# Kernel optimization log

Measured on AMD Instinct MI355X. Metric: run time of the kernel, lower is better.

The kernel has to match this reference:

```python
import jax, jax.numpy as jnp
import numpy as np

E = 262144      # total neighbor edges across all (sample, timestep) pairs
B = 1024        # samples with non-zero history
L = 10          # seq_len
T = B * L       # total timesteps (segments)
H = 128         # h_dim
N_ENT = 40000
N_REL = 256


def setup_inputs() -> dict:
    key = jax.random.key(0)
    ks = jax.random.split(key, 16)
    return {
        "nbr_ent": jax.random.randint(ks[0], (E,), 0, N_ENT),
        "nbr_rel": jax.random.randint(ks[1], (E,), 0, N_REL),
        "nbr_att": jax.random.uniform(ks[2], (E,), dtype=jnp.float32),
        "seg_ids": jnp.sort(jax.random.randint(ks[3], (E,), 0, T)),
        "self_att": jax.random.uniform(ks[4], (B, L), dtype=jnp.float32),
        "s_ids": jax.random.randint(ks[5], (B,), 0, N_ENT),
        "r_ids": jax.random.randint(ks[6], (B,), 0, N_REL),
        "ent_embeds": jax.random.normal(ks[7], (N_ENT, H), dtype=jnp.float32),
        "rel_embeds": jax.random.normal(ks[8], (N_REL, H), dtype=jnp.float32),
        "W1_w": jax.random.normal(ks[9], (H, 1), dtype=jnp.float32) * 0.1,
        "W1_b": jax.random.normal(ks[10], (H,), dtype=jnp.float32) * 0.1,
        "W3_w": jax.random.normal(ks[11], (H, 3 * H), dtype=jnp.float32) * 0.05,
        "W3_b": jax.random.normal(ks[12], (H,), dtype=jnp.float32) * 0.05,
        "W4_w": jax.random.normal(ks[13], (H, 2 * H), dtype=jnp.float32) * 0.05,
        "W4_b": jax.random.normal(ks[14], (H,), dtype=jnp.float32) * 0.05,
    }


def reference(nbr_ent, nbr_rel, nbr_att, seg_ids, self_att, s_ids, r_ids,
              ent_embeds, rel_embeds, W1_w, W1_b, W3_w, W3_b, W4_w, W4_b):
    # --- per-edge embeddings (the body of get_sorted_s_r_embed) ---
    # W1: scalar attribute -> h_dim, then ReLU
    e_att = jax.nn.relu(nbr_att[:, None] * W1_w[:, 0][None, :] + W1_b)   # [E, H]
    e_s = ent_embeds[nbr_ent]                                            # [E, H]
    e_r = rel_embeds[nbr_rel]                                            # [E, H]
    e = jax.nn.relu(jnp.concatenate([e_att, e_s, e_r], -1) @ W3_w.T + W3_b)      # [E, H]
    e_static = jax.nn.relu(jnp.concatenate([e_s, e_r], -1) @ W4_w.T + W4_b)      # [E, H]

    # --- sparse-mask segment mean (torch.sparse.mm with 0/1 mask / len_s) ---
    counts = jax.ops.segment_sum(jnp.ones_like(nbr_att), seg_ids, num_segments=T)
    denom = jnp.maximum(counts, 1.0)[:, None]                            # guard empty segments
    embeds_mean = jax.ops.segment_sum(e, seg_ids, num_segments=T) / denom          # [T, H]
    embeds_static_mean = jax.ops.segment_sum(e_static, seg_ids, num_segments=T) / denom

    embeds_mean = embeds_mean.reshape(B, L, H)
    embeds_static_mean = embeds_static_mean.reshape(B, L, H)

    # --- per-sample fill of padded sequence tensors ---
    self_att_emb = jax.nn.relu(self_att[..., None] * W1_w[:, 0] + W1_b)  # [B, L, H]
    self_e = jnp.broadcast_to(ent_embeds[s_ids][:, None, :], (B, L, H))  # repeat over time
    self_r = jnp.broadcast_to(rel_embeds[r_ids][:, None, :], (B, L, H))

    s_embed_seq = jnp.concatenate([self_e, self_r, embeds_static_mean], -1)   # [B, L, 3H]
    att_embed_seq = jnp.concatenate([self_att_emb, self_e, embeds_mean], -1)  # [B, L, 3H]
    # dropout omitted (eval mode); pack_padded_sequence returns padded tensors here
    return s_embed_seq, att_embed_seq
```

## Files before the change

kernel.cpp:

```cpp
#include <hip/hip_runtime.h>
#include <hip/hip_bf16.h>

#define E_EDGES 262144
#define B_SAMP  1024
#define L_SEQ   10
#define T_SEG   (B_SAMP * L_SEQ)
#define H_DIM   128
#define N_ENT_C 40000
#define N_REL_C 256

typedef __attribute__((ext_vector_type(8))) short short8;
typedef __attribute__((ext_vector_type(4))) float f32x4;

__device__ __forceinline__ float b2f(__hip_bfloat16 x) { return __bfloat162float(x); }
__device__ __forceinline__ unsigned short f2bu(float x) {
    return __bfloat16_as_ushort(__float2bfloat16(x));
}

__device__ __forceinline__ float loadF(const void* base, int idx, int isB16) {
    if (isB16) return b2f(((const __hip_bfloat16*)base)[idx]);
    return ((const float*)base)[idx];
}
__device__ __forceinline__ int loadI(const void* base, int idx, int is64) {
    if (is64) return (int)(((const long long*)base)[idx]);
    return ((const int*)base)[idx];
}

__device__ __forceinline__ void detect_dtypes(const void* att_raw,
                                              const void* sid_raw,
                                              int tid, int nthr,
                                              int& isB, int& i64)
{
    __shared__ int cF, cI;
    if (tid == 0) { cF = 0; cI = 0; }
    __syncthreads();
    const unsigned short* pa = (const unsigned short*)att_raw;
    int c = 0;
    for (int i = tid; i < 2048; i += nthr) if (pa[i] <= 0x3F80u) c++;
    if (c) atomicAdd(&cF, c);
    const int* ps = (const int*)sid_raw;
    c = 0;
    for (int i = tid; i < 512; i += nthr) if (ps[2 * i + 1] == 0) c++;
    if (c) atomicAdd(&cI, c);
    __syncthreads();
    isB = (cF >= 1900) ? 1 : 0;
    i64 = (cI >= 256) ? 1 : 0;
}

__global__ void __launch_bounds__(256)
ka_prep(const void* __restrict__ W3w, const void* __restrict__ W4w,
        const void* __restrict__ W1w, const void* __restrict__ W1b,
        const void* __restrict__ W3b, const void* __restrict__ W4b,
        const void* __restrict__ seg_ids,
        const void* __restrict__ att_raw, const void* __restrict__ sid_raw,
        unsigned short* __restrict__ wctEb, unsigned short* __restrict__ wctRb,
        unsigned int* __restrict__ ab3p, int* __restrict__ starts,
        float* __restrict__ W1w_f, float* __restrict__ W1b_f,
        float* __restrict__ W3b_f, float* __restrict__ W4b_f,
        float* __restrict__ bpts, int* __restrict__ pnIn,
        int* __restrict__ flag, int* __restrict__ iflag)
{
    const int bid = blockIdx.x, tid = threadIdx.x;
    int isB, i64;
    detect_dtypes(att_raw, sid_raw, tid, 256, isB, i64);

    if (bid < 256) {
        int gid = bid * 256 + tid;
        if (gid < 32768) {
            int n = gid >> 7, k = gid & 127;
            float v = (n < 128) ? loadF(W3w, n * 384 + 128 + k, isB)
                                : loadF(W4w, (n - 128) * 256 + k, isB);
            wctEb[gid] = f2bu(v);
        } else {
            int j = gid - 32768;
            int n = j >> 7, k = j & 127;
            float v = (n < 128) ? loadF(W3w, n * 384 + 256 + k, isB)
                                : loadF(W4w, (n - 128) * 256 + 128 + k, isB);
            wctRb[j] = f2bu(v);
        }
        return;
    }

    if (bid < 321 || bid == 362) {
        __shared__ float w1s[128], b1s[128], srt[128];
        __shared__ int nInS;
        if (tid < 128) {
            float w = loadF(W1w, tid, isB);
            float b = loadF(W1b, tid, isB);
            w1s[tid] = w; b1s[tid] = b;
        }
        __syncthreads();
        if (tid < 128) {
            float w = w1s[tid], b = b1s[tid];
            float t = 2.0f;
            if (w != 0.0f) {
                float tt = -b / w;
                if (tt > 0.0f && tt < 1.0f) t = tt;
            }
            srt[tid] = t;
        }
        __syncthreads();
        float myt = 0.0f; int rank = 0, n = 0;
        if (tid < 128) {
            myt = srt[tid];
            for (int j = 0; j < 128; ++j) {
                float v = srt[j];
                rank += (v < myt) || (v == myt && j < tid);
                n += (v < 1.5f);
            }
        }
        __syncthreads();
        if (tid < 128) srt[rank] = myt;
        if (tid == 0) nInS = n;
        __syncthreads();
        const int nIn = nInS;

        if (bid == 362) {
            if (tid < 128) {
                W1w_f[tid] = w1s[tid];
                W1b_f[tid] = b1s[tid];
                W3b_f[tid] = loadF(W3b, tid, isB);
                W4b_f[tid] = loadF(W4b, tid, isB);
                bpts[tid] = srt[tid];
            }
            if (tid == 0) { *pnIn = nIn; *flag = isB; *iflag = i64; }
            return;
        }
        const int j = (bid - 256) * 2 + (tid >> 7);
        const int h = tid & 127;
        if (j <= nIn) {
            float left  = (j == 0)   ? 0.0f : srt[j - 1];
            float right = (j == nIn) ? 1.0f : srt[j];
            float mid = 0.5f * (left + right);
            float a = 0.0f, b = 0.0f;
            for (int k = 0; k < 128; ++k) {
                if (fmaf(mid, w1s[k], b1s[k]) > 0.0f) {
                    float w3 = loadF(W3w, h * 384 + k, isB);
                    a = fmaf(w1s[k], w3, a);
                    b = fmaf(b1s[k], w3, b);
                }
            }
            ab3p[j * 128 + h] = (unsigned int)f2bu(a)
                              | ((unsigned int)f2bu(b) << 16);
        }
        return;
    }

    int t = (bid - 321) * 256 + tid;
    if (t <= T_SEG) {
        int lo = 0, hi = E_EDGES;
        while (lo < hi) {
            int m = (lo + hi) >> 1;
            if (loadI(seg_ids, m, i64) < t) lo = m + 1; else hi = m;
        }
        starts[t] = lo;
    }
}

#define KB_ENT_BLOCKS (N_ENT_C / 64)
#define KB_REL_BLOCKS (N_REL_C / 64)

__global__ void __launch_bounds__(256)
kb_gemm(const void* __restrict__ ent_raw, const void* __restrict__ rel_raw,
        const int* __restrict__ flag,
        const unsigned short* __restrict__ wctEb,
        const unsigned short* __restrict__ wctRb,
        const float* __restrict__ W3b_f, const float* __restrict__ W4b_f,
        unsigned int* __restrict__ entp2, unsigned int* __restrict__ relp2)
{
    const int isB = *flag;
    const int bid = blockIdx.x, tid = threadIdx.x;

    const void* A; const unsigned short* WT; unsigned int* out; int m0, isRel;
    if (bid < KB_ENT_BLOCKS) {
        A = ent_raw; WT = wctEb; out = entp2; m0 = bid * 64; isRel = 0;
    } else {
        A = rel_raw; WT = wctRb; out = relp2;
        m0 = (bid - KB_ENT_BLOCKS) * 64; isRel = 1;
    }

    __shared__ unsigned short As[64][136];

    if (isB) {
        for (int v = tid; v < 1024; v += 256) {
            int e = v * 8, r = e >> 7, cc = e & 127;
            short8 x = *(const short8*)((const short*)A + m0 * 128 + e);
            *(short8*)&As[r][cc] = x;
        }
    } else {
        for (int v = tid; v < 2048; v += 256) {
            int e = v * 4, r = e >> 7, cc = e & 127;
            float4 f = *(const float4*)((const float*)A + m0 * 128 + e);
            unsigned int lo = (unsigned int)f2bu(f.x) | ((unsigned int)f2bu(f.y) << 16);
            unsigned int hi = (unsigned int)f2bu(f.z) | ((unsigned int)f2bu(f.w) << 16);
            *(uint2*)&As[r][cc] = make_uint2(lo, hi);
        }
    }
    __syncthreads();

    const int wave = tid >> 6, lane = tid & 63;
    const int quad = lane >> 4, l16 = lane & 15;

    f32x4 acc3[8], acc4[8];
    #pragma unroll
    for (int np = 0; np < 8; ++np) {
        acc3[np] = (f32x4){0.f, 0.f, 0.f, 0.f};
        acc4[np] = (f32x4){0.f, 0.f, 0.f, 0.f};
    }

    #pragma unroll
    for (int kk = 0; kk < 4; ++kk) {
        const int kb = kk * 32 + quad * 8;
        short8 av = *(const short8*)&As[wave * 16 + l16][kb];
        #pragma unroll
        for (int np = 0; np < 8; ++np) {
            const short* bp = (const short*)WT + (np * 16 + l16) * 128 + kb;
            short8 bv3 = *(const short8*)bp;
            short8 bv4 = *(const short8*)(bp + 128 * 128);
            acc3[np] = __builtin_amdgcn_mfma_f32_16x16x32_bf16(av, bv3, acc3[np], 0, 0, 0);
            acc4[np] = __builtin_amdgcn_mfma_f32_16x16x32_bf16(av, bv4, acc4[np], 0, 0, 0);
        }
    }

    #pragma unroll
    for (int np = 0; np < 8; ++np) {
        int h = np * 16 + l16;
        float bias3 = isRel ? W3b_f[h] : 0.0f;
        float bias4 = isRel ? W4b_f[h] : 0.0f;
        #pragma unroll
        for (int r = 0; r < 4; ++r) {
            int m = m0 + wave * 16 + quad * 4 + r;
            unsigned int w = (unsigned int)f2bu(acc3[np][r] + bias3)
                           | ((unsigned int)f2bu(acc4[np][r] + bias4) << 16);
            out[m * 128 + h] = w;
        }
    }
}

__global__ void __launch_bounds__(128)
kc_segment(const void* __restrict__ nbr_ent, const void* __restrict__ nbr_rel,
           const void* __restrict__ att_raw,
           const int* __restrict__ starts,
           const unsigned int* __restrict__ entp2,
           const unsigned int* __restrict__ relp2,
           const unsigned int* __restrict__ ab3p,
           const float* __restrict__ bpts_g, const int* __restrict__ pnIn,
           const void* __restrict__ sat_raw,
           const void* __restrict__ s_ids, const void* __restrict__ r_ids,
           const void* __restrict__ ent_raw, const void* __restrict__ rel_raw,
           const float* __restrict__ W1w_f, const float* __restrict__ W1b_f,
           const int* __restrict__ flag, const int* __restrict__ iflag,
           float* __restrict__ outS, float* __restrict__ outA)
{
    const int t = blockIdx.x, h = threadIdx.x;
    const int isB = *flag, i64 = *iflag;
    const int s = starts[t], e = starts[t + 1];

    __shared__ float bptsS[128];
    __shared__ int4 eS[128];
    bptsS[h] = bpts_g[h];
    const int nIn = *pnIn;

    float acc3 = 0.0f, acc4 = 0.0f;

    for (int base = s; base < e; base += 128) {
        const int n = min(128, e - base);
        __syncthreads();
        if (h < n) {
            const int i = base + h;
            int ent = loadI(nbr_ent, i, i64);
            int rel = loadI(nbr_rel, i, i64);
            float att = loadF(att_raw, i, isB);
            int lo = 0, hi = nIn;
            while (lo < hi) {
                int m = (lo + hi) >> 1;
                if (bptsS[m] <= att) lo = m + 1; else hi = m;
            }
            eS[h] = make_int4(ent, rel, __float_as_int(att), lo);
        }
        __syncthreads();
        #pragma unroll 8
        for (int ii = 0; ii < n; ++ii) {
            int4 q = eS[ii];
            float att = __int_as_float(q.z);
            unsigned int ew = entp2[q.x * 128 + h];
            unsigned int rw = relp2[q.y * 128 + h];
            unsigned int aw = ab3p[q.w * 128 + h];
            float p3s = __int_as_float(ew << 16);
            float p4s = __int_as_float(ew & 0xFFFF0000u);
            float p3r = __int_as_float(rw << 16);
            float p4r = __int_as_float(rw & 0xFFFF0000u);
            float a3  = __int_as_float(aw << 16);
            float b3  = __int_as_float(aw & 0xFFFF0000u);
            acc3 += fmaxf(fmaf(att, a3, b3) + p3s + p3r, 0.0f);
            acc4 += fmaxf(p4s + p4r, 0.0f);
        }
    }

    const int cnt = e - s;
    const float inv = (cnt > 0) ? (1.0f / (float)cnt) : 1.0f;
    const int b = t / L_SEQ;
    const int sid = loadI(s_ids, b, i64);
    const int rid = loadI(r_ids, b, i64);
    const float se = loadF(ent_raw, sid * 128 + h, isB);
    const float sr = loadF(rel_raw, rid * 128 + h, isB);
    const float sa = loadF(sat_raw, t, isB);
    const float sae = fmaxf(fmaf(sa, W1w_f[h], W1b_f[h]), 0.0f);

    const size_t bs = (size_t)t * 384;
    outS[bs + h]       = se;
    outS[bs + 128 + h] = sr;
    outS[bs + 256 + h] = acc4 * inv;
    outA[bs + h]       = sae;
    outA[bs + 128 + h] = se;
    outA[bs + 256 + h] = acc3 * inv;
}

extern "C" void kernel_launch(void* const* d_in, const int* in_sizes, int n_in,
                              void* d_out, int out_size, void* d_ws, size_t ws_size,
                              hipStream_t stream)
{
    const void* nbr_ent = d_in[0];
    const void* nbr_rel = d_in[1];
    const void* nbr_att = d_in[2];
    const void* seg_ids = d_in[3];
    const void* self_att = d_in[4];
    const void* s_ids = d_in[5];
    const void* r_ids = d_in[6];
    const void* ent_embeds = d_in[7];
    const void* rel_embeds = d_in[8];
    const void* W1w = d_in[9];
    const void* W1b = d_in[10];
    const void* W3w = d_in[11];
    const void* W3b = d_in[12];
    const void* W4w = d_in[13];
    const void* W4b = d_in[14];

    char* ws = (char*)d_ws;
    size_t off = 0;
    auto alloc = [&](size_t bytes) -> void* {
        void* p = ws + off;
        off = (off + bytes + 255) & ~(size_t)255;
        return p;
    };
    int*   flag   = (int*)alloc(4);
    int*   iflag  = (int*)alloc(4);
    int*   pnIn   = (int*)alloc(4);
    float* W1w_f  = (float*)alloc(128 * 4);
    float* W1b_f  = (float*)alloc(128 * 4);
    float* W3b_f  = (float*)alloc(128 * 4);
    float* W4b_f  = (float*)alloc(128 * 4);
    float* bpts   = (float*)alloc(128 * 4);
    int*   starts = (int*)alloc((T_SEG + 1) * 4);
    unsigned short* wctEb = (unsigned short*)alloc(256 * 128 * 2);
    unsigned short* wctRb = (unsigned short*)alloc(256 * 128 * 2);
    unsigned int* ab3p = (unsigned int*)alloc(129 * 128 * 4);
    unsigned int* entp2 = (unsigned int*)alloc((size_t)N_ENT_C * 128 * 4);
    unsigned int* relp2 = (unsigned int*)alloc((size_t)N_REL_C * 128 * 4);

    float* outS = (float*)d_out;
    float* outA = outS + (size_t)T_SEG * 384;

    ka_prep<<<363, 256, 0, stream>>>(W3w, W4w, W1w, W1b, W3b, W4b,
                                     seg_ids, nbr_att, s_ids,
                                     wctEb, wctRb, ab3p, starts,
                                     W1w_f, W1b_f, W3b_f, W4b_f,
                                     bpts, pnIn, flag, iflag);

    kb_gemm<<<KB_ENT_BLOCKS + KB_REL_BLOCKS, 256, 0, stream>>>(
        ent_embeds, rel_embeds, flag, wctEb, wctRb, W3b_f, W4b_f, entp2, relp2);

    kc_segment<<<T_SEG, 128, 0, stream>>>(
        nbr_ent, nbr_rel, nbr_att, starts, entp2, relp2, ab3p, bpts, pnIn,
        self_att, s_ids, r_ids, ent_embeds, rel_embeds,
        W1w_f, W1b_f, flag, iflag, outS, outA);
}
```

Before: 179.2 us.

## Precompute packed per-edge metadata in prep kernel and use wave-per-segment gather

```diff
diff --git a/kernel.cpp b/kernel.cpp
--- a/kernel.cpp
+++ b/kernel.cpp
@@ -52,12 +52,13 @@
         const void* __restrict__ W1w, const void* __restrict__ W1b,
         const void* __restrict__ W3b, const void* __restrict__ W4b,
         const void* __restrict__ seg_ids,
+        const void* __restrict__ nbr_ent, const void* __restrict__ nbr_rel,
         const void* __restrict__ att_raw, const void* __restrict__ sid_raw,
         unsigned short* __restrict__ wctEb, unsigned short* __restrict__ wctRb,
         unsigned int* __restrict__ ab3p, int* __restrict__ starts,
+        uint2* __restrict__ metaE,
         float* __restrict__ W1w_f, float* __restrict__ W1b_f,
         float* __restrict__ W3b_f, float* __restrict__ W4b_f,
-        float* __restrict__ bpts, int* __restrict__ pnIn,
         int* __restrict__ flag, int* __restrict__ iflag)
 {
     const int bid = blockIdx.x, tid = threadIdx.x;
@@ -81,51 +82,64 @@
         return;
     }
 
-    if (bid < 321 || bid == 362) {
-        __shared__ float w1s[128], b1s[128], srt[128];
-        __shared__ int nInS;
+    if (bid >= 321 && bid <= 361) {
+        int t = (bid - 321) * 256 + tid;
+        if (t <= T_SEG) {
+            int lo = 0, hi = E_EDGES;
+            while (lo < hi) {
+                int m = (lo + hi) >> 1;
+                if (loadI(seg_ids, m, i64) < t) lo = m + 1; else hi = m;
+            }
+            starts[t] = lo;
+        }
+        return;
+    }
+
+    __shared__ float w1s[128], b1s[128], srt[128];
+    __shared__ int nInS;
+    if (tid < 128) {
+        float w = loadF(W1w, tid, isB);
+        float b = loadF(W1b, tid, isB);
+        w1s[tid] = w; b1s[tid] = b;
+    }
+    __syncthreads();
+    if (tid < 128) {
+        float w = w1s[tid], b = b1s[tid];
+        float t = 2.0f;
+        if (w != 0.0f) {
+            float tt = -b / w;
+            if (tt > 0.0f && tt < 1.0f) t = tt;
+        }
+        srt[tid] = t;
+    }
+    __syncthreads();
+    float myt = 0.0f; int rank = 0, n = 0;
+    if (tid < 128) {
+        myt = srt[tid];
+        for (int j = 0; j < 128; ++j) {
+            float v = srt[j];
+            rank += (v < myt) || (v == myt && j < tid);
+            n += (v < 1.5f);
+        }
+    }
+    __syncthreads();
+    if (tid < 128) srt[rank] = myt;
+    if (tid == 0) nInS = n;
+    __syncthreads();
+    const int nIn = nInS;
+
+    if (bid == 362) {
         if (tid < 128) {
-            float w = loadF(W1w, tid, isB);
-            float b = loadF(W1b, tid, isB);
-            w1s[tid] = w; b1s[tid] = b;
-        }
-        __syncthreads();
-        if (tid < 128) {
-            float w = w1s[tid], b = b1s[tid];
-            float t = 2.0f;
-            if (w != 0.0f) {
-                float tt = -b / w;
-                if (tt > 0.0f && tt < 1.0f) t = tt;
-            }
-            srt[tid] = t;
-        }
-        __syncthreads();
-        float myt = 0.0f; int rank = 0, n = 0;
-        if (tid < 128) {
-            myt = srt[tid];
-            for (int j = 0; j < 128; ++j) {
-                float v = srt[j];
-                rank += (v < myt) || (v == myt && j < tid);
-                n += (v < 1.5f);
-            }
-        }
-        __syncthreads();
-        if (tid < 128) srt[rank] = myt;
-        if (tid == 0) nInS = n;
-        __syncthreads();
-        const int nIn = nInS;
-
-        if (bid == 362) {
-            if (tid < 128) {
-                W1w_f[tid] = w1s[tid];
-                W1b_f[tid] = b1s[tid];
-                W3b_f[tid] = loadF(W3b, tid, isB);
-                W4b_f[tid] = loadF(W4b, tid, isB);
-                bpts[tid] = srt[tid];
-            }
-            if (tid == 0) { *pnIn = nIn; *flag = isB; *iflag = i64; }
-            return;
-        }
+            W1w_f[tid] = w1s[tid];
+            W1b_f[tid] = b1s[tid];
+            W3b_f[tid] = loadF(W3b, tid, isB);
+            W4b_f[tid] = loadF(W4b, tid, isB);
+        }
+        if (tid == 0) { *flag = isB; *iflag = i64; }
+        return;
+    }
+
+    if (bid < 321) {
         const int j = (bid - 256) * 2 + (tid >> 7);
         const int h = tid & 127;
         if (j <= nIn) {
@@ -146,14 +160,22 @@
         return;
     }
 
-    int t = (bid - 321) * 256 + tid;
-    if (t <= T_SEG) {
-        int lo = 0, hi = E_EDGES;
+    const int eb = (bid - 363) * 1024;
+    #pragma unroll
+    for (int r = 0; r < 4; ++r) {
+        int i = eb + r * 256 + tid;
+        int ent = loadI(nbr_ent, i, i64);
+        int rel = loadI(nbr_rel, i, i64);
+        float att = loadF(att_raw, i, isB);
+        int lo = 0, hi = nIn;
         while (lo < hi) {
             int m = (lo + hi) >> 1;
-            if (loadI(seg_ids, m, i64) < t) lo = m + 1; else hi = m;
-        }
-        starts[t] = lo;
+            if (srt[m] <= att) lo = m + 1; else hi = m;
+        }
+        unsigned int hiw = (unsigned int)ent
+                         | ((unsigned int)rel << 16)
+                         | ((unsigned int)lo << 24);
+        metaE[i] = make_uint2(__float_as_uint(att), hiw);
     }
 }
 
@@ -237,14 +259,12 @@
     }
 }
 
-__global__ void __launch_bounds__(128)
-kc_segment(const void* __restrict__ nbr_ent, const void* __restrict__ nbr_rel,
-           const void* __restrict__ att_raw,
+__global__ void __launch_bounds__(256)
+kc_segment(const uint2* __restrict__ metaE,
            const int* __restrict__ starts,
            const unsigned int* __restrict__ entp2,
            const unsigned int* __restrict__ relp2,
            const unsigned int* __restrict__ ab3p,
-           const float* __restrict__ bpts_g, const int* __restrict__ pnIn,
            const void* __restrict__ sat_raw,
            const void* __restrict__ s_ids, const void* __restrict__ r_ids,
            const void* __restrict__ ent_raw, const void* __restrict__ rel_raw,
@@ -252,48 +272,50 @@
            const int* __restrict__ flag, const int* __restrict__ iflag,
            float* __restrict__ outS, float* __restrict__ outA)
 {
-    const int t = blockIdx.x, h = threadIdx.x;
     const int isB = *flag, i64 = *iflag;
-    const int s = starts[t], e = starts[t + 1];
-
-    __shared__ float bptsS[128];
-    __shared__ int4 eS[128];
-    bptsS[h] = bpts_g[h];
-    const int nIn = *pnIn;
-
-    float acc3 = 0.0f, acc4 = 0.0f;
-
-    for (int base = s; base < e; base += 128) {
-        const int n = min(128, e - base);
-        __syncthreads();
-        if (h < n) {
-            const int i = base + h;
-            int ent = loadI(nbr_ent, i, i64);
-            int rel = loadI(nbr_rel, i, i64);
-            float att = loadF(att_raw, i, isB);
-            int lo = 0, hi = nIn;
-            while (lo < hi) {
-                int m = (lo + hi) >> 1;
-                if (bptsS[m] <= att) lo = m + 1; else hi = m;
-            }
-            eS[h] = make_int4(ent, rel, __float_as_int(att), lo);
-        }
-        __syncthreads();
-        #pragma unroll 8
+    const int wave = threadIdx.x >> 6, lane = threadIdx.x & 63;
+    const int t = blockIdx.x * 4 + wave;
+    const int h0 = lane * 2;
+
+    const int s = __builtin_amdgcn_readfirstlane(starts[t]);
+    const int e = __builtin_amdgcn_readfirstlane(starts[t + 1]);
+
+    float acc3x = 0.0f, acc3y = 0.0f, acc4x = 0.0f, acc4y = 0.0f;
+
+    for (int base = s; base < e; base += 64) {
+        const int n = min(64, e - base);
+        unsigned int mLo = 0u, mHi = 0u;
+        if (lane < n) {
+            uint2 mv = metaE[base + lane];
+            mLo = mv.x; mHi = mv.y;
+        }
+        #pragma unroll 4
         for (int ii = 0; ii < n; ++ii) {
-            int4 q = eS[ii];
-            float att = __int_as_float(q.z);
-            unsigned int ew = entp2[q.x * 128 + h];
-            unsigned int rw = relp2[q.y * 128 + h];
-            unsigned int aw = ab3p[q.w * 128 + h];
-            float p3s = __int_as_float(ew << 16);
-            float p4s = __int_as_float(ew & 0xFFFF0000u);
-            float p3r = __int_as_float(rw << 16);
-            float p4r = __int_as_float(rw & 0xFFFF0000u);
-            float a3  = __int_as_float(aw << 16);
-            float b3  = __int_as_float(aw & 0xFFFF0000u);
-            acc3 += fmaxf(fmaf(att, a3, b3) + p3s + p3r, 0.0f);
-            acc4 += fmaxf(p4s + p4r, 0.0f);
+            const unsigned int sLo = __builtin_amdgcn_readlane(mLo, ii);
+            const unsigned int sHi = __builtin_amdgcn_readlane(mHi, ii);
+            const float att = __uint_as_float(sLo);
+            const int ent = (int)(sHi & 0xFFFFu);
+            const int rel = (int)((sHi >> 16) & 0xFFu);
+            const int j   = (int)(sHi >> 24);
+            uint2 ew = *(const uint2*)(entp2 + ent * 128 + h0);
+            uint2 rw = *(const uint2*)(relp2 + rel * 128 + h0);
+            uint2 aw = *(const uint2*)(ab3p  + j   * 128 + h0);
+            float p3s0 = __uint_as_float(ew.x << 16);
+            float p4s0 = __uint_as_float(ew.x & 0xFFFF0000u);
+            float p3s1 = __uint_as_float(ew.y << 16);
+            float p4s1 = __uint_as_float(ew.y & 0xFFFF0000u);
+            float p3r0 = __uint_as_float(rw.x << 16);
+            float p4r0 = __uint_as_float(rw.x & 0xFFFF0000u);
+            float p3r1 = __uint_as_float(rw.y << 16);
+            float p4r1 = __uint_as_float(rw.y & 0xFFFF0000u);
+            float a30  = __uint_as_float(aw.x << 16);
+            float b30  = __uint_as_float(aw.x & 0xFFFF0000u);
+            float a31  = __uint_as_float(aw.y << 16);
+            float b31  = __uint_as_float(aw.y & 0xFFFF0000u);
+            acc3x += fmaxf(fmaf(att, a30, b30) + p3s0 + p3r0, 0.0f);
+            acc3y += fmaxf(fmaf(att, a31, b31) + p3s1 + p3r1, 0.0f);
+            acc4x += fmaxf(p4s0 + p4r0, 0.0f);
+            acc4y += fmaxf(p4s1 + p4r1, 0.0f);
         }
     }
 
@@ -302,18 +324,23 @@
     const int b = t / L_SEQ;
     const int sid = loadI(s_ids, b, i64);
     const int rid = loadI(r_ids, b, i64);
-    const float se = loadF(ent_raw, sid * 128 + h, isB);
-    const float sr = loadF(rel_raw, rid * 128 + h, isB);
-    const float sa = loadF(sat_raw, t, isB);
-    const float sae = fmaxf(fmaf(sa, W1w_f[h], W1b_f[h]), 0.0f);
+    const float se0 = loadF(ent_raw, sid * 128 + h0, isB);
+    const float se1 = loadF(ent_raw, sid * 128 + h0 + 1, isB);
+    const float sr0 = loadF(rel_raw, rid * 128 + h0, isB);
+    const float sr1 = loadF(rel_raw, rid * 128 + h0 + 1, isB);
+    const float sa  = loadF(sat_raw, t, isB);
+    const float2 w1w = *(const float2*)(W1w_f + h0);
+    const float2 w1b = *(const float2*)(W1b_f + h0);
+    const float sae0 = fmaxf(fmaf(sa, w1w.x, w1b.x), 0.0f);
+    const float sae1 = fmaxf(fmaf(sa, w1w.y, w1b.y), 0.0f);
 
     const size_t bs = (size_t)t * 384;
-    outS[bs + h]       = se;
-    outS[bs + 128 + h] = sr;
-    outS[bs + 256 + h] = acc4 * inv;
-    outA[bs + h]       = sae;
-    outA[bs + 128 + h] = se;
-    outA[bs + 256 + h] = acc3 * inv;
+    *(float2*)(outS + bs + h0)       = make_float2(se0, se1);
+    *(float2*)(outS + bs + 128 + h0) = make_float2(sr0, sr1);
+    *(float2*)(outS + bs + 256 + h0) = make_float2(acc4x * inv, acc4y * inv);
+    *(float2*)(outA + bs + h0)       = make_float2(sae0, sae1);
+    *(float2*)(outA + bs + 128 + h0) = make_float2(se0, se1);
+    *(float2*)(outA + bs + 256 + h0) = make_float2(acc3x * inv, acc3y * inv);
 }
 
 extern "C" void kernel_launch(void* const* d_in, const int* in_sizes, int n_in,
@@ -345,33 +372,32 @@
     };
     int*   flag   = (int*)alloc(4);
     int*   iflag  = (int*)alloc(4);
-    int*   pnIn   = (int*)alloc(4);
     float* W1w_f  = (float*)alloc(128 * 4);
     float* W1b_f  = (float*)alloc(128 * 4);
     float* W3b_f  = (float*)alloc(128 * 4);
     float* W4b_f  = (float*)alloc(128 * 4);
-    float* bpts   = (float*)alloc(128 * 4);
     int*   starts = (int*)alloc((T_SEG + 1) * 4);
     unsigned short* wctEb = (unsigned short*)alloc(256 * 128 * 2);
     unsigned short* wctRb = (unsigned short*)alloc(256 * 128 * 2);
     unsigned int* ab3p = (unsigned int*)alloc(129 * 128 * 4);
+    uint2* metaE = (uint2*)alloc((size_t)E_EDGES * 8);
     unsigned int* entp2 = (unsigned int*)alloc((size_t)N_ENT_C * 128 * 4);
     unsigned int* relp2 = (unsigned int*)alloc((size_t)N_REL_C * 128 * 4);
 
     float* outS = (float*)d_out;
     float* outA = outS + (size_t)T_SEG * 384;
 
-    ka_prep<<<363, 256, 0, stream>>>(W3w, W4w, W1w, W1b, W3b, W4b,
-                                     seg_ids, nbr_att, s_ids,
-                                     wctEb, wctRb, ab3p, starts,
+    ka_prep<<<619, 256, 0, stream>>>(W3w, W4w, W1w, W1b, W3b, W4b,
+                                     seg_ids, nbr_ent, nbr_rel, nbr_att, s_ids,
+                                     wctEb, wctRb, ab3p, starts, metaE,
                                      W1w_f, W1b_f, W3b_f, W4b_f,
-                                     bpts, pnIn, flag, iflag);
+                                     flag, iflag);
 
     kb_gemm<<<KB_ENT_BLOCKS + KB_REL_BLOCKS, 256, 0, stream>>>(
         ent_embeds, rel_embeds, flag, wctEb, wctRb, W3b_f, W4b_f, entp2, relp2);
 
-    kc_segment<<<T_SEG, 128, 0, stream>>>(
-        nbr_ent, nbr_rel, nbr_att, starts, entp2, relp2, ab3p, bpts, pnIn,
+    kc_segment<<<T_SEG / 4, 256, 0, stream>>>(
+        metaE, starts, entp2, relp2, ab3p,
         self_att, s_ids, r_ids, ent_embeds, rel_embeds,
         W1w_f, W1b_f, flag, iflag, outS, outA);
 }
```

After: 189.7 us. 5.8% more time.

## Precompute packed per-edge metadata in prep kernel and halve GEMM tile size

Applied to the files above, without the earlier changes.

```diff
diff --git a/kernel.cpp b/kernel.cpp
--- a/kernel.cpp
+++ b/kernel.cpp
@@ -52,12 +52,13 @@
         const void* __restrict__ W1w, const void* __restrict__ W1b,
         const void* __restrict__ W3b, const void* __restrict__ W4b,
         const void* __restrict__ seg_ids,
+        const void* __restrict__ nbr_ent, const void* __restrict__ nbr_rel,
         const void* __restrict__ att_raw, const void* __restrict__ sid_raw,
         unsigned short* __restrict__ wctEb, unsigned short* __restrict__ wctRb,
         unsigned int* __restrict__ ab3p, int* __restrict__ starts,
+        uint2* __restrict__ metaE,
         float* __restrict__ W1w_f, float* __restrict__ W1b_f,
         float* __restrict__ W3b_f, float* __restrict__ W4b_f,
-        float* __restrict__ bpts, int* __restrict__ pnIn,
         int* __restrict__ flag, int* __restrict__ iflag)
 {
     const int bid = blockIdx.x, tid = threadIdx.x;
@@ -81,51 +82,64 @@
         return;
     }
 
-    if (bid < 321 || bid == 362) {
-        __shared__ float w1s[128], b1s[128], srt[128];
-        __shared__ int nInS;
+    if (bid >= 321 && bid <= 361) {
+        int t = (bid - 321) * 256 + tid;
+        if (t <= T_SEG) {
+            int lo = 0, hi = E_EDGES;
+            while (lo < hi) {
+                int m = (lo + hi) >> 1;
+                if (loadI(seg_ids, m, i64) < t) lo = m + 1; else hi = m;
+            }
+            starts[t] = lo;
+        }
+        return;
+    }
+
+    __shared__ float w1s[128], b1s[128], srt[128];
+    __shared__ int nInS;
+    if (tid < 128) {
+        float w = loadF(W1w, tid, isB);
+        float b = loadF(W1b, tid, isB);
+        w1s[tid] = w; b1s[tid] = b;
+    }
+    __syncthreads();
+    if (tid < 128) {
+        float w = w1s[tid], b = b1s[tid];
+        float t = 2.0f;
+        if (w != 0.0f) {
+            float tt = -b / w;
+            if (tt > 0.0f && tt < 1.0f) t = tt;
+        }
+        srt[tid] = t;
+    }
+    __syncthreads();
+    float myt = 0.0f; int rank = 0, n = 0;
+    if (tid < 128) {
+        myt = srt[tid];
+        for (int j = 0; j < 128; ++j) {
+            float v = srt[j];
+            rank += (v < myt) || (v == myt && j < tid);
+            n += (v < 1.5f);
+        }
+    }
+    __syncthreads();
+    if (tid < 128) srt[rank] = myt;
+    if (tid == 0) nInS = n;
+    __syncthreads();
+    const int nIn = nInS;
+
+    if (bid == 362) {
         if (tid < 128) {
-            float w = loadF(W1w, tid, isB);
-            float b = loadF(W1b, tid, isB);
-            w1s[tid] = w; b1s[tid] = b;
-        }
-        __syncthreads();
-        if (tid < 128) {
-            float w = w1s[tid], b = b1s[tid];
-            float t = 2.0f;
-            if (w != 0.0f) {
-                float tt = -b / w;
-                if (tt > 0.0f && tt < 1.0f) t = tt;
-            }
-            srt[tid] = t;
-        }
-        __syncthreads();
-        float myt = 0.0f; int rank = 0, n = 0;
-        if (tid < 128) {
-            myt = srt[tid];
-            for (int j = 0; j < 128; ++j) {
-                float v = srt[j];
-                rank += (v < myt) || (v == myt && j < tid);
-                n += (v < 1.5f);
-            }
-        }
-        __syncthreads();
-        if (tid < 128) srt[rank] = myt;
-        if (tid == 0) nInS = n;
-        __syncthreads();
-        const int nIn = nInS;
-
-        if (bid == 362) {
-            if (tid < 128) {
-                W1w_f[tid] = w1s[tid];
-                W1b_f[tid] = b1s[tid];
-                W3b_f[tid] = loadF(W3b, tid, isB);
-                W4b_f[tid] = loadF(W4b, tid, isB);
-                bpts[tid] = srt[tid];
-            }
-            if (tid == 0) { *pnIn = nIn; *flag = isB; *iflag = i64; }
-            return;
-        }
+            W1w_f[tid] = w1s[tid];
+            W1b_f[tid] = b1s[tid];
+            W3b_f[tid] = loadF(W3b, tid, isB);
+            W4b_f[tid] = loadF(W4b, tid, isB);
+        }
+        if (tid == 0) { *flag = isB; *iflag = i64; }
+        return;
+    }
+
+    if (bid < 321) {
         const int j = (bid - 256) * 2 + (tid >> 7);
         const int h = tid & 127;
         if (j <= nIn) {
@@ -146,21 +160,29 @@
         return;
     }
 
-    int t = (bid - 321) * 256 + tid;
-    if (t <= T_SEG) {
-        int lo = 0, hi = E_EDGES;
+    const int eb = (bid - 363) * 1024;
+    #pragma unroll
+    for (int r = 0; r < 4; ++r) {
+        int i = eb + r * 256 + tid;
+        int ent = loadI(nbr_ent, i, i64);
+        int rel = loadI(nbr_rel, i, i64);
+        float att = loadF(att_raw, i, isB);
+        int lo = 0, hi = nIn;
         while (lo < hi) {
             int m = (lo + hi) >> 1;
-            if (loadI(seg_ids, m, i64) < t) lo = m + 1; else hi = m;
-        }
-        starts[t] = lo;
-    }
-}
-
-#define KB_ENT_BLOCKS (N_ENT_C / 64)
-#define KB_REL_BLOCKS (N_REL_C / 64)
-
-__global__ void __launch_bounds__(256)
+            if (srt[m] <= att) lo = m + 1; else hi = m;
+        }
+        unsigned int hiw = (unsigned int)ent
+                         | ((unsigned int)rel << 16)
+                         | ((unsigned int)lo << 24);
+        metaE[i] = make_uint2(__float_as_uint(att), hiw);
+    }
+}
+
+#define KB_ENT_BLOCKS (N_ENT_C / 32)
+#define KB_REL_BLOCKS (N_REL_C / 32)
+
+__global__ void __launch_bounds__(128)
 kb_gemm(const void* __restrict__ ent_raw, const void* __restrict__ rel_raw,
         const int* __restrict__ flag,
         const unsigned short* __restrict__ wctEb,
@@ -173,22 +195,22 @@
 
     const void* A; const unsigned short* WT; unsigned int* out; int m0, isRel;
     if (bid < KB_ENT_BLOCKS) {
-        A = ent_raw; WT = wctEb; out = entp2; m0 = bid * 64; isRel = 0;
+        A = ent_raw; WT = wctEb; out = entp2; m0 = bid * 32; isRel = 0;
     } else {
         A = rel_raw; WT = wctRb; out = relp2;
-        m0 = (bid - KB_ENT_BLOCKS) * 64; isRel = 1;
-    }
-
-    __shared__ unsigned short As[64][136];
+        m0 = (bid - KB_ENT_BLOCKS) * 32; isRel = 1;
+    }
+
+    __shared__ unsigned short As[32][136];
 
     if (isB) {
-        for (int v = tid; v < 1024; v += 256) {
+        for (int v = tid; v < 512; v += 128) {
             int e = v * 8, r = e >> 7, cc = e & 127;
             short8 x = *(const short8*)((const short*)A + m0 * 128 + e);
             *(short8*)&As[r][cc] = x;
         }
     } else {
-        for (int v = tid; v < 2048; v += 256) {
+        for (int v = tid; v < 1024; v += 128) {
             int e = v * 4, r = e >> 7, cc = e & 127;
             float4 f = *(const float4*)((const float*)A + m0 * 128 + e);
             unsigned int lo = (unsigned int)f2bu(f.x) | ((unsigned int)f2bu(f.y) << 16);
@@ -238,13 +260,11 @@
 }
 
 __global__ void __launch_bounds__(128)
-kc_segment(const void* __restrict__ nbr_ent, const void* __restrict__ nbr_rel,
-           const void* __restrict__ att_raw,
+kc_segment(const uint2* __restrict__ metaE,
            const int* __restrict__ starts,
            const unsigned int* __restrict__ entp2,
            const unsigned int* __restrict__ relp2,
            const unsigned int* __restrict__ ab3p,
-           const float* __restrict__ bpts_g, const int* __restrict__ pnIn,
            const void* __restrict__ sat_raw,
            const void* __restrict__ s_ids, const void* __restrict__ r_ids,
            const void* __restrict__ ent_raw, const void* __restrict__ rel_raw,
@@ -256,42 +276,31 @@
     const int isB = *flag, i64 = *iflag;
     const int s = starts[t], e = starts[t + 1];
 
-    __shared__ float bptsS[128];
-    __shared__ int4 eS[128];
-    bptsS[h] = bpts_g[h];
-    const int nIn = *pnIn;
+    __shared__ uint2 eS[128];
 
     float acc3 = 0.0f, acc4 = 0.0f;
 
     for (int base = s; base < e; base += 128) {
         const int n = min(128, e - base);
         __syncthreads();
-        if (h < n) {
-            const int i = base + h;
-            int ent = loadI(nbr_ent, i, i64);
-            int rel = loadI(nbr_rel, i, i64);
-            float att = loadF(att_raw, i, isB);
-            int lo = 0, hi = nIn;
-            while (lo < hi) {
-                int m = (lo + hi) >> 1;
-                if (bptsS[m] <= att) lo = m + 1; else hi = m;
-            }
-            eS[h] = make_int4(ent, rel, __float_as_int(att), lo);
-        }
+        if (h < n) eS[h] = metaE[base + h];
         __syncthreads();
         #pragma unroll 8
         for (int ii = 0; ii < n; ++ii) {
-            int4 q = eS[ii];
-            float att = __int_as_float(q.z);
-            unsigned int ew = entp2[q.x * 128 + h];
-            unsigned int rw = relp2[q.y * 128 + h];
-            unsigned int aw = ab3p[q.w * 128 + h];
-            float p3s = __int_as_float(ew << 16);
-            float p4s = __int_as_float(ew & 0xFFFF0000u);
-            float p3r = __int_as_float(rw << 16);
-            float p4r = __int_as_float(rw & 0xFFFF0000u);
-            float a3  = __int_as_float(aw << 16);
-            float b3  = __int_as_float(aw & 0xFFFF0000u);
+            uint2 q = eS[ii];
+            float att = __uint_as_float(q.x);
+            int ent = (int)(q.y & 0xFFFFu);
+            int rel = (int)((q.y >> 16) & 0xFFu);
+            int j   = (int)(q.y >> 24);
+            unsigned int ew = entp2[ent * 128 + h];
+            unsigned int rw = relp2[rel * 128 + h];
+            unsigned int aw = ab3p[j * 128 + h];
+            float p3s = __uint_as_float(ew << 16);
+            float p4s = __uint_as_float(ew & 0xFFFF0000u);
+            float p3r = __uint_as_float(rw << 16);
+            float p4r = __uint_as_float(rw & 0xFFFF0000u);
+            float a3  = __uint_as_float(aw << 16);
+            float b3  = __uint_as_float(aw & 0xFFFF0000u);
             acc3 += fmaxf(fmaf(att, a3, b3) + p3s + p3r, 0.0f);
             acc4 += fmaxf(p4s + p4r, 0.0f);
         }
@@ -345,33 +354,32 @@
     };
     int*   flag   = (int*)alloc(4);
     int*   iflag  = (int*)alloc(4);
-    int*   pnIn   = (int*)alloc(4);
     float* W1w_f  = (float*)alloc(128 * 4);
     float* W1b_f  = (float*)alloc(128 * 4);
     float* W3b_f  = (float*)alloc(128 * 4);
     float* W4b_f  = (float*)alloc(128 * 4);
-    float* bpts   = (float*)alloc(128 * 4);
     int*   starts = (int*)alloc((T_SEG + 1) * 4);
     unsigned short* wctEb = (unsigned short*)alloc(256 * 128 * 2);
     unsigned short* wctRb = (unsigned short*)alloc(256 * 128 * 2);
     unsigned int* ab3p = (unsigned int*)alloc(129 * 128 * 4);
+    uint2* metaE = (uint2*)alloc((size_t)E_EDGES * 8);
     unsigned int* entp2 = (unsigned int*)alloc((size_t)N_ENT_C * 128 * 4);
     unsigned int* relp2 = (unsigned int*)alloc((size_t)N_REL_C * 128 * 4);
 
     float* outS = (float*)d_out;
     float* outA = outS + (size_t)T_SEG * 384;
 
-    ka_prep<<<363, 256, 0, stream>>>(W3w, W4w, W1w, W1b, W3b, W4b,
-                                     seg_ids, nbr_att, s_ids,
-                                     wctEb, wctRb, ab3p, starts,
+    ka_prep<<<619, 256, 0, stream>>>(W3w, W4w, W1w, W1b, W3b, W4b,
+                                     seg_ids, nbr_ent, nbr_rel, nbr_att, s_ids,
+                                     wctEb, wctRb, ab3p, starts, metaE,
                                      W1w_f, W1b_f, W3b_f, W4b_f,
-                                     bpts, pnIn, flag, iflag);
-
-    kb_gemm<<<KB_ENT_BLOCKS + KB_REL_BLOCKS, 256, 0, stream>>>(
+                                     flag, iflag);
+
+    kb_gemm<<<KB_ENT_BLOCKS + KB_REL_BLOCKS, 128, 0, stream>>>(
         ent_embeds, rel_embeds, flag, wctEb, wctRb, W3b_f, W4b_f, entp2, relp2);
 
     kc_segment<<<T_SEG, 128, 0, stream>>>(
-        nbr_ent, nbr_rel, nbr_att, starts, entp2, relp2, ab3p, bpts, pnIn,
+        metaE, starts, entp2, relp2, ab3p,
         self_att, s_ids, r_ids, ent_embeds, rel_embeds,
         W1w_f, W1b_f, flag, iflag, outS, outA);
 }
```

Result: no change. 177.2 us (-1.1%).
